# Performance work log

Hardware: AMD Instinct MI355X
Metric: run time of the kernel (lower is better)

Reference implementation:

```python
import jax, jax.numpy as jnp
import numpy as np

B = 2048        # batch
D_IN = 512      # input_dim
H = 768         # hidden_dim
A = 5001        # num_atoms
RULE_LEN = 4
N_DATA = 56000.0


def setup_inputs() -> dict:
    key = jax.random.key(0)
    ks = jax.random.split(key, 24)
    def w(k, shape, fan):
        return (jax.random.normal(k, shape, jnp.float32) / np.sqrt(fan)).astype(jnp.float32)
    return {
        'x': jax.random.normal(ks[0], (B, D_IN), jnp.float32),
        'x_mask': jax.random.randint(ks[1], (B, A), 0, 2, jnp.int32),
        # linear_base: Linear(512,768) ReLU Linear(768,768) ReLU Linear(768,768)
        'W1': w(ks[2], (H, D_IN), D_IN), 'b1': jnp.zeros((H,), jnp.float32),
        'W2': w(ks[3], (H, H), H),       'b2': jnp.zeros((H,), jnp.float32),
        'W3': w(ks[4], (H, H), H),       'b3': jnp.zeros((H,), jnp.float32),
        # single-layer GRU (input H, hidden H); gates ordered r,z,n as in torch
        'W_ih': w(ks[5], (3 * H, H), H), 'b_ih': jnp.zeros((3 * H,), jnp.float32),
        'W_hh': w(ks[6], (3 * H, H), H), 'b_hh': jnp.zeros((3 * H,), jnp.float32),
        # gru_head: Linear(H, num_atoms)
        'Wh': w(ks[7], (A, H), H), 'bh': jnp.zeros((A,), jnp.float32),
        # atom embedding table
        'ae_weight': jax.random.normal(ks[8], (A, H), jnp.float32) * 0.02,
        # stand-in consequent estimator heads (mu, coverage)
        'w_mu': w(ks[9], (H, 1), H),  'b_mu': jnp.zeros((1,), jnp.float32),
        'w_cov': w(ks[10], (H, 1), H), 'b_cov': jnp.zeros((1,), jnp.float32),
        'alpha': jnp.ones((1,), jnp.float32),
    }


def _gru_step(xt, h, W_ih, b_ih, W_hh, b_hh):
    gi = xt @ W_ih.T + b_ih
    gh = h @ W_hh.T + b_hh
    i_r, i_z, i_n = jnp.split(gi, 3, axis=-1)
    h_r, h_z, h_n = jnp.split(gh, 3, axis=-1)
    r = jax.nn.sigmoid(i_r + h_r)
    z = jax.nn.sigmoid(i_z + h_z)
    n = jnp.tanh(i_n + r * h_n)
    return (1.0 - z) * n + z * h


def reference(x, x_mask, W1, b1, W2, b2, W3, b3, W_ih, b_ih, W_hh, b_hh,
              Wh, bh, ae_weight, w_mu, b_mu, w_cov, b_cov, alpha):
    # base (dnn) encoder -> cls embedding [B, H]
    cls = jax.nn.relu(x @ W1.T + b1)
    cls = jax.nn.relu(cls @ W2.T + b2)
    cls = cls @ W3.T + b3

    ae_det = jax.lax.stop_gradient(ae_weight)  # ae.weight is always detached in the original
    mask = x_mask.astype(jnp.float32)
    h = jnp.zeros_like(cls)
    cur = cls
    probs = []
    idx = None
    gkey = jax.random.key(42)
    batch_idx = jnp.arange(cls.shape[0])

    for j in range(RULE_LEN):
        h = _gru_step(cur, h, W_ih, b_ih, W_hh, b_hh)  # dropout = identity (eval)
        logits = h @ Wh.T + bh  # [B, A]
        if j == 0:
            row_zero = jnp.sum(mask, axis=1) == 0.0
            mask = mask.at[:, 0].set(jnp.where(row_zero, 1.0, mask[:, 0]))
        else:
            mask = jnp.where((idx == 0)[:, None], 0.0, mask)
            mask = mask.at[:, 0].set(1.0)
        masked = jnp.where(mask > 0.0, logits, -jnp.inf)
        # gumbel-softmax, tau=1, hard=True (straight-through)
        u = jax.random.uniform(jax.random.fold_in(gkey, j), masked.shape,
                               jnp.float32, 1e-6, 1.0 - 1e-6)
        g = -jnp.log(-jnp.log(u))
        y_soft = jax.nn.softmax(masked + g, axis=1)
        idx = jnp.argmax(y_soft, axis=1)
        y_hard = jax.nn.one_hot(idx, A, dtype=y_soft.dtype)
        prob = y_hard + y_soft - jax.lax.stop_gradient(y_soft)
        probs.append(prob)
        # scatter zero at the selected atom so it can't repeat
        mask = mask.at[batch_idx, idx].set(0.0)
        cur = cls + prob @ ae_det  # [B, H]

    atom_prob = jnp.stack(probs, axis=1)  # [B, rule_len, A]
    atoms = jnp.einsum('bra,ad->brd', atom_prob, ae_det)  # [B, rule_len, H]

    # stand-in consequent estimator: (mu, coverage) from summed atoms
    a = jnp.sum(atoms, axis=1)
    mu = jax.nn.sigmoid(a @ w_mu + b_mu)[:, 0]
    coverage = jax.nn.sigmoid(a @ w_cov + b_cov)[:, 0]

    n = coverage * N_DATA
    inv = alpha[0] / n
    pp = (mu + inv) / (1.0 + 2.0 * inv)
    cp = jnp.stack([1.0 - pp, pp], axis=-1)  # [B, 2]
    out = jnp.log(cp)  # head=1 -> mean over heads is identity
    return (out, atom_prob, cp)
```

## Files before the change

kernel.cpp:

```cpp
#include <hip/hip_runtime.h>
#include <stdint.h>
#include <math.h>

#define B_    2048
#define DIN_  512
#define H_    768
#define G3_   2304
#define A_    5001
#define APAD_ 5120
#define RL_   4
#define NDATA_ 56000.0f

typedef _Float16 f16x8 __attribute__((ext_vector_type(8)));
typedef _Float16 f16x4 __attribute__((ext_vector_type(4)));
typedef float    f32x4 __attribute__((ext_vector_type(4)));

__host__ __device__ __forceinline__ void threefry2x32(
    uint32_t k0, uint32_t k1, uint32_t x0, uint32_t x1,
    uint32_t* o0, uint32_t* o1)
{
  const uint32_t ks2 = k0 ^ k1 ^ 0x1BD11BDAu;
#define TF_R(r) { x0 += x1; x1 = (x1 << (r)) | (x1 >> (32 - (r))); x1 ^= x0; }
  x0 += k0; x1 += k1;
  TF_R(13) TF_R(15) TF_R(26) TF_R(6)
  x0 += k1;  x1 += ks2 + 1u;
  TF_R(17) TF_R(29) TF_R(16) TF_R(24)
  x0 += ks2; x1 += k0 + 2u;
  TF_R(13) TF_R(15) TF_R(26) TF_R(6)
  x0 += k0;  x1 += k1 + 3u;
  TF_R(17) TF_R(29) TF_R(16) TF_R(24)
  x0 += k1;  x1 += ks2 + 4u;
  TF_R(13) TF_R(15) TF_R(26) TF_R(6)
  x0 += ks2; x1 += k0 + 5u;
#undef TF_R
  *o0 = x0; *o1 = x1;
}

__device__ __forceinline__ float gumbel_for(uint32_t k0, uint32_t k1, uint32_t n)
{
  uint32_t o0, o1;
  threefry2x32(k0, k1, 0u, n, &o0, &o1);
  const uint32_t bits = o0 ^ o1;
  const float f = __uint_as_float((bits >> 9) | 0x3f800000u);
  const float minv = 1e-6f;
  const float maxv = 1.0f - 1e-6f;
  const float span = maxv - minv;
  float u = __fmul_rn(f, span);
  u = __fadd_rn(u, minv);
  u = __fsub_rn(u, span);
  u = fmaxf(minv, u);
  return -logf(-logf(u));
}

struct HL { _Float16 h, l; };
__device__ __forceinline__ HL split64(float v)
{
  HL r;
  const float s = v * 64.f;
  r.h = (_Float16)s;
  r.l = (_Float16)(s - (float)r.h);
  return r;
}

__device__ __forceinline__ void gload16(const void* g, void* l)
{
  __builtin_amdgcn_global_load_lds(
      (const __attribute__((address_space(1))) void*)g,
      (__attribute__((address_space(3))) void*)l, 16, 0, 0);
}

struct PSJobs {
  const float* src[7];
  _Float16* hi[7];
  _Float16* lo[7];
  int R[7]; int K[7]; int trans[7];
  int cum[8];
};

__global__ __launch_bounds__(256)
void presplit_all(PSJobs J)
{
  const int g = blockIdx.x * 256 + threadIdx.x;
  if (g >= J.cum[7]) return;
  int j = 0;
  while (g >= J.cum[j + 1]) ++j;
  const int i = g - J.cum[j];
  const int K = J.K[j];
  const int e = i * 4;
  const int row = e / K;
  const int col = e - row * K;
  float4 f = make_float4(0.f, 0.f, 0.f, 0.f);
  if (J.trans[j]) {
    const int R = J.R[j];
    f.x = J.src[j][(size_t)(col + 0) * R + row];
    f.y = J.src[j][(size_t)(col + 1) * R + row];
    f.z = J.src[j][(size_t)(col + 2) * R + row];
    f.w = J.src[j][(size_t)(col + 3) * R + row];
  } else if (row < J.R[j]) {
    f = *(const float4*)(J.src[j] + (size_t)row * K + col);
  }
  const HL s0 = split64(f.x), s1 = split64(f.y);
  const HL s2 = split64(f.z), s3 = split64(f.w);
  const f16x4 hv = {s0.h, s1.h, s2.h, s3.h};
  ((f16x4*)J.hi[j])[i] = hv;
  if (J.lo[j]) {
    const f16x4 lv = {s0.l, s1.l, s2.l, s3.l};
    ((f16x4*)J.lo[j])[i] = lv;
  }
}

__global__ __launch_bounds__(256)
void prep_k(const int* __restrict__ xmask, uint8_t* __restrict__ mask,
            const float* __restrict__ Wh, float* __restrict__ wmaxsq,
            const float* __restrict__ x, _Float16* __restrict__ xh,
            _Float16* __restrict__ xl, const float* __restrict__ Wih,
            const float* __restrict__ b3, const float* __restrict__ bih,
            float* __restrict__ bprime)
{
  const int blk = blockIdx.x, tid = threadIdx.x;
  const int XB = (B_ * DIN_ / 4 + 255) / 256;
  __shared__ float redf[256];
  __shared__ int   redi[256];
  if (blk < B_) {
    const int b = blk;
    int s = 0;
    for (int a = tid; a < A_; a += 256) {
      const int m = (xmask[(size_t)b * A_ + a] != 0) ? 1 : 0;
      mask[(size_t)b * A_ + a] = (uint8_t)m;
      s += m;
    }
    redi[tid] = s; __syncthreads();
    for (int t = 128; t > 0; t >>= 1) {
      if (tid < t) redi[tid] += redi[tid + t];
      __syncthreads();
    }
    if (tid == 0 && redi[0] == 0) mask[(size_t)b * A_] = 1;
  } else if (blk < B_ + A_) {
    const int a = blk - B_;
    float p = 0.f;
    for (int d = tid; d < H_; d += 256) {
      const float w = Wh[(size_t)a * H_ + d];
      p += w * w;
    }
    redf[tid] = p; __syncthreads();
    for (int t = 128; t > 0; t >>= 1) {
      if (tid < t) redf[tid] += redf[tid + t];
      __syncthreads();
    }
    if (tid == 0) atomicMax((int*)wmaxsq, __float_as_int(redf[0]));
  } else if (blk < B_ + A_ + XB) {
    const int i = (blk - B_ - A_) * 256 + tid;
    const int n4 = B_ * DIN_ / 4;
    if (i < n4) {
      const float4 f = ((const float4*)x)[i];
      const HL s0 = split64(f.x), s1 = split64(f.y);
      const HL s2 = split64(f.z), s3 = split64(f.w);
      const f16x4 hv = {s0.h, s1.h, s2.h, s3.h};
      const f16x4 lv = {s0.l, s1.l, s2.l, s3.l};
      ((f16x4*)xh)[i] = hv;
      ((f16x4*)xl)[i] = lv;
    }
  } else {
    const int n = blk - B_ - A_ - XB;
    float p = 0.f;
    for (int d = tid; d < H_; d += 256)
      p += Wih[(size_t)n * H_ + d] * b3[d];
    redf[tid] = p; __syncthreads();
    for (int t = 128; t > 0; t >>= 1) {
      if (tid < t) redf[tid] += redf[tid + t];
      __syncthreads();
    }
    if (tid == 0) bprime[n] = redf[0] + bih[n];
  }
}

struct GJob {
  const _Float16 *Ah, *Al, *Bh, *Bl;
  const float* bias;
  float* C;
  _Float16 *Ch, *Cl;
  int M, K, ldc, n0, Nv;
  int npass, act, wsplit, gum;
};
struct GArgs { GJob j[3]; int sx1, sx2; uint32_t k0, k1; };

__global__ __launch_bounds__(256)
void gemm2job(GArgs P)
{
  __shared__ _Float16 sA[2][128 * 32];
  __shared__ _Float16 sB[2][128 * 32];

  const int bx = blockIdx.x;
  const int jid = (bx < P.sx1) ? 0 : ((bx < P.sx2) ? 1 : 2);
  const GJob J = P.j[jid];
  const int bxx = bx - ((jid == 0) ? 0 : ((jid == 1) ? P.sx1 : P.sx2));
  const int bm = blockIdx.y * 128;
  if (bm >= J.M) return;
  const int bn = J.n0 + bxx * 128;

  const int tid = threadIdx.x;
  const int lane = tid & 63, wave = tid >> 6;
  const int wx = wave & 1, wy = wave >> 1;
  const int q = lane >> 4, mr = lane & 15;
  const int K = J.K;
  const int np3 = (J.npass == 3);

  f32x4 acc[4][4];
#pragma unroll
  for (int i = 0; i < 4; ++i)
#pragma unroll
    for (int j = 0; j < 4; ++j) acc[i][j] = (f32x4)0.f;

  const int abase = (wy * 64 + mr) * 32 + q * 8;
  const int bbase = (wx * 64 + mr) * 32 + q * 8;

  if (np3) {
    auto stage = [&](int k0) {
#pragma unroll
      for (int t = 0; t < 2; ++t) {
        const int c = wave * 2 + t;
        const int row = c * 16 + (lane >> 2);
        const int kc = (lane & 3) * 8;
        const size_t ga = (size_t)(bm + row) * K + k0 + kc;
        const size_t gb = (size_t)(bn + row) * K + k0 + kc;
        gload16(J.Ah + ga, &sA[0][c * 512]);
        gload16(J.Bh + gb, &sB[0][c * 512]);
        gload16(J.Al + ga, &sA[1][c * 512]);
        gload16(J.Bl + gb, &sB[1][c * 512]);
      }
    };
    stage(0);
    const int T = K / 32;
    for (int t = 0; t < T; ++t) {
      __syncthreads();
      f16x8 ah[4], al[4], bhv[4], blv[4];
#pragma unroll
      for (int mi = 0; mi < 4; ++mi) {
        ah[mi]  = *(const f16x8*)&sA[0][abase + mi * 512];
        bhv[mi] = *(const f16x8*)&sB[0][bbase + mi * 512];
        al[mi]  = *(const f16x8*)&sA[1][abase + mi * 512];
        blv[mi] = *(const f16x8*)&sB[1][bbase + mi * 512];
      }
      __syncthreads();
      if (t + 1 < T) stage((t + 1) * 32);
#pragma unroll
      for (int ni = 0; ni < 4; ++ni)
#pragma unroll
        for (int mi = 0; mi < 4; ++mi) {
          acc[mi][ni] = __builtin_amdgcn_mfma_f32_16x16x32_f16(ah[mi], bhv[ni], acc[mi][ni], 0, 0, 0);
          acc[mi][ni] = __builtin_amdgcn_mfma_f32_16x16x32_f16(al[mi], bhv[ni], acc[mi][ni], 0, 0, 0);
          acc[mi][ni] = __builtin_amdgcn_mfma_f32_16x16x32_f16(ah[mi], blv[ni], acc[mi][ni], 0, 0, 0);
        }
    }
  } else {
    auto stage64 = [&](int k0) {
#pragma unroll
      for (int t = 0; t < 2; ++t) {
        const int c = wave * 2 + t;
        const int row = c * 16 + (lane >> 2);
        const int kc = (lane & 3) * 8;
        const size_t ga = (size_t)(bm + row) * K + k0 + kc;
        const size_t gb = (size_t)(bn + row) * K + k0 + kc;
        gload16(J.Ah + ga, &sA[0][c * 512]);
        gload16(J.Bh + gb, &sB[0][c * 512]);
        gload16(J.Ah + ga + 32, &sA[1][c * 512]);
        gload16(J.Bh + gb + 32, &sB[1][c * 512]);
      }
    };
    stage64(0);
    const int T2 = K / 64;
    for (int t = 0; t < T2; ++t) {
      __syncthreads();
      f16x8 a0[4], b0[4];
#pragma unroll
      for (int mi = 0; mi < 4; ++mi) {
        a0[mi] = *(const f16x8*)&sA[0][abase + mi * 512];
        b0[mi] = *(const f16x8*)&sB[0][bbase + mi * 512];
      }
#pragma unroll
      for (int ni = 0; ni < 4; ++ni)
#pragma unroll
        for (int mi = 0; mi < 4; ++mi)
          acc[mi][ni] = __builtin_amdgcn_mfma_f32_16x16x32_f16(a0[mi], b0[ni], acc[mi][ni], 0, 0, 0);
      f16x8 a1[4], b1[4];
#pragma unroll
      for (int mi = 0; mi < 4; ++mi) {
        a1[mi] = *(const f16x8*)&sA[1][abase + mi * 512];
        b1[mi] = *(const f16x8*)&sB[1][bbase + mi * 512];
      }
      __syncthreads();
      if (t + 1 < T2) stage64((t + 1) * 64);
#pragma unroll
      for (int ni = 0; ni < 4; ++ni)
#pragma unroll
        for (int mi = 0; mi < 4; ++mi)
          acc[mi][ni] = __builtin_amdgcn_mfma_f32_16x16x32_f16(a1[mi], b1[ni], acc[mi][ni], 0, 0, 0);
    }
  }

  const float sc = 1.f / 4096.f;
#pragma unroll
  for (int ni = 0; ni < 4; ++ni) {
    const int n = bn + wx * 64 + ni * 16 + mr;
    if (n >= J.Nv) continue;
    const float bv = J.bias ? J.bias[n] : 0.f;
#pragma unroll
    for (int mi = 0; mi < 4; ++mi) {
      const int m0 = bm + wy * 64 + mi * 16 + q * 4;
#pragma unroll
      for (int r = 0; r < 4; ++r) {
        const int m = m0 + r;
        float v = acc[mi][ni][r] * sc + bv;
        if (J.act) v = fmaxf(v, 0.f);
        if (J.gum) v += gumbel_for(P.k0, P.k1, (uint32_t)(m * J.ldc + n));
        const size_t off = (size_t)m * J.ldc + n;
        if (J.C) J.C[off] = v;
        if (J.wsplit) {
          const HL s = split64(v);
          J.Ch[off] = s.h;
          J.Cl[off] = s.l;
        }
      }
    }
  }
}

__global__ __launch_bounds__(256)
void gru_elem(const float* __restrict__ gi, const float* __restrict__ bhh,
              float* __restrict__ h, _Float16* __restrict__ hh_,
              _Float16* __restrict__ hl_)
{
  const int i = blockIdx.x * 256 + threadIdx.x;
  if (i >= B_ * H_) return;
  const int b = i / H_;
  const int d = i - b * H_;
  const float* gib = gi + (size_t)b * G3_;
  const float ir = gib[d], iz = gib[H_ + d], in_ = gib[2 * H_ + d];
  const float hr = bhh[d], hz = bhh[H_ + d], hn = bhh[2 * H_ + d];
  const float r = 1.f / (1.f + expf(-(ir + hr)));
  const float z = 1.f / (1.f + expf(-(iz + hz)));
  const float n = tanhf(in_ + r * hn);
  const float hv = (1.f - z) * n;
  h[i] = hv;
  const HL s = split64(hv);
  hh_[i] = s.h; hl_[i] = s.l;
}

__global__ __launch_bounds__(256)
void select_step(const float* __restrict__ v, uint8_t* __restrict__ mask,
                 int* __restrict__ idxs, const float* __restrict__ giCls,
                 const float* __restrict__ AeWih, float* __restrict__ atomp,
                 float* __restrict__ hbuf, const float* __restrict__ WhF,
                 const float* __restrict__ bh, const float* __restrict__ wmaxsq,
                 const float* __restrict__ gh, const float* __restrict__ bhh,
                 _Float16* __restrict__ hh_, _Float16* __restrict__ hl_,
                 uint32_t k0, uint32_t k1, int step)
{
  const int b = blockIdx.x, tid = threadIdx.x;
  uint8_t* mrow = mask + (size_t)b * A_;
  __shared__ float hsh[H_];
  __shared__ float sv[256];
  __shared__ int   si[256];
  __shared__ int   s_list[64];
  __shared__ int   s_n;
  __shared__ int   s_sel;

  float hp = 0.f;
  for (int d = tid; d < H_; d += 256) {
    const float t = hbuf[(size_t)b * H_ + d];
    hsh[d] = t; hp += t * t;
  }
  sv[tid] = hp; __syncthreads();
  for (int t = 128; t > 0; t >>= 1) {
    if (tid < t) sv[tid] += sv[tid + t];
    __syncthreads();
  }
  const float hn2 = sv[0];
  __syncthreads();

  if (step > 0) {
    const int prev = idxs[(step - 1) * B_ + b];
    if (prev == 0)
      for (int a = tid; a < A_; a += 256) mrow[a] = 0;
    __syncthreads();
    if (tid == 0) mrow[0] = 1;
  }
  if (tid == 0) s_n = 0;
  __syncthreads();

  const float* vrow = v + (size_t)b * A_;
  float bv = -INFINITY; int bi = A_;
  for (int a = tid; a < A_; a += 256) {
    const float val = mrow[a] ? vrow[a] : -INFINITY;
    if (val > bv) { bv = val; bi = a; }
  }
  sv[tid] = bv; si[tid] = bi; __syncthreads();
  for (int t = 128; t > 0; t >>= 1) {
    if (tid < t) {
      const float v2 = sv[tid + t]; const int i2 = si[tid + t];
      if (v2 > sv[tid] || (v2 == sv[tid] && i2 < si[tid])) { sv[tid] = v2; si[tid] = i2; }
    }
    __syncthreads();
  }
  const float amax = sv[0];
  __syncthreads();

  const float delta = 2.0f * 0.0009765625f * sqrtf(hn2 * wmaxsq[0]);
  const float thr = amax - 2.f * delta;

  for (int a = tid; a < A_; a += 256)
    if (mrow[a] && vrow[a] >= thr) {
      const int p = atomicAdd(&s_n, 1);
      if (p < 64) s_list[p] = a;
    }
  __syncthreads();
  const int nc = (s_n < 64) ? s_n : 64;

  const uint32_t nbase = (uint32_t)b * (uint32_t)A_;
  float best = -INFINITY; int bestA = A_;
  for (int c = 0; c < nc; ++c) {
    const int a = s_list[c];
    const float* wr = WhF + (size_t)a * H_;
    float p = 0.f;
    for (int d = tid; d < H_; d += 256) p += hsh[d] * wr[d];
    sv[tid] = p; __syncthreads();
    for (int t = 128; t > 0; t >>= 1) {
      if (tid < t) sv[tid] += sv[tid + t];
      __syncthreads();
    }
    if (tid == 0) {
      const float ev = sv[0] + bh[a] + gumbel_for(k0, k1, nbase + (uint32_t)a);
      if (ev > best || (ev == best && a < bestA)) { best = ev; bestA = a; }
    }
    __syncthreads();
  }
  if (tid == 0) {
    s_sel = bestA;
    mrow[bestA] = 0;
    idxs[step * B_ + b] = bestA;
    atomp[(size_t)b * (RL_ * A_) + (size_t)step * A_ + bestA] = 1.0f;
  }
  __syncthreads();

  if (step < RL_ - 1) {
    const int sel = s_sel;
    const float* ar = AeWih + (size_t)sel * G3_;
    const float* gr = giCls + (size_t)b * G3_;
    const float* ghb = gh + (size_t)b * G3_;
    for (int d = tid; d < H_; d += 256) {
      const float g0 = gr[d] + ar[d];
      const float g1 = gr[H_ + d] + ar[H_ + d];
      const float g2 = gr[2 * H_ + d] + ar[2 * H_ + d];
      const float r = 1.f / (1.f + expf(-(g0 + ghb[d])));
      const float z = 1.f / (1.f + expf(-(g1 + ghb[H_ + d])));
      const float n = tanhf(g2 + r * ghb[2 * H_ + d]);
      const float hv = (1.f - z) * n + z * hsh[d];
      hbuf[(size_t)b * H_ + d] = hv;
      const HL s = split64(hv);
      hh_[(size_t)b * H_ + d] = s.h;
      hl_[(size_t)b * H_ + d] = s.l;
    }
  }
}

__global__ __launch_bounds__(256)
void head_k(const int* __restrict__ idxs, const float* __restrict__ ae,
            const float* __restrict__ w_mu, const float* __restrict__ b_mu,
            const float* __restrict__ w_cov, const float* __restrict__ b_cov,
            const float* __restrict__ alpha, float* __restrict__ outf)
{
  const int b = blockIdx.x, tid = threadIdx.x;
  const int i0 = idxs[0 * B_ + b], i1 = idxs[1 * B_ + b];
  const int i2 = idxs[2 * B_ + b], i3 = idxs[3 * B_ + b];
  const float* r0 = ae + (size_t)i0 * H_;
  const float* r1 = ae + (size_t)i1 * H_;
  const float* r2 = ae + (size_t)i2 * H_;
  const float* r3 = ae + (size_t)i3 * H_;
  float pmu = 0.f, pcv = 0.f;
  for (int d = tid; d < H_; d += 256) {
    const float a = r0[d] + r1[d] + r2[d] + r3[d];
    pmu += a * w_mu[d];
    pcv += a * w_cov[d];
  }
  __shared__ float smu[256], scv[256];
  smu[tid] = pmu; scv[tid] = pcv;
  __syncthreads();
  for (int s = 128; s > 0; s >>= 1) {
    if (tid < s) { smu[tid] += smu[tid + s]; scv[tid] += scv[tid + s]; }
    __syncthreads();
  }
  if (tid == 0) {
    const float mu = 1.f / (1.f + expf(-(smu[0] + b_mu[0])));
    const float cv = 1.f / (1.f + expf(-(scv[0] + b_cov[0])));
    const float n = cv * NDATA_;
    const float inv = alpha[0] / n;
    const float pp = (mu + inv) / (1.f + 2.f * inv);
    outf[2 * b + 0] = logf(1.f - pp);
    outf[2 * b + 1] = logf(pp);
    float* cp = outf + 2 * B_ + (size_t)B_ * RL_ * A_;
    cp[2 * b + 0] = 1.f - pp;
    cp[2 * b + 1] = pp;
  }
}

extern "C" void kernel_launch(void* const* d_in, const int* in_sizes, int n_in,
                              void* d_out, int out_size, void* d_ws, size_t ws_size,
                              hipStream_t stream)
{
  const float* x     = (const float*)d_in[0];
  const int*   xmask = (const int*)d_in[1];
  const float* W1 = (const float*)d_in[2];  const float* b1 = (const float*)d_in[3];
  const float* W2 = (const float*)d_in[4];  const float* b2 = (const float*)d_in[5];
  const float* W3 = (const float*)d_in[6];  const float* b3 = (const float*)d_in[7];
  const float* Wih = (const float*)d_in[8]; const float* bih = (const float*)d_in[9];
  const float* Whh = (const float*)d_in[10];const float* bhh = (const float*)d_in[11];
  const float* Wh = (const float*)d_in[12]; const float* bh = (const float*)d_in[13];
  const float* ae = (const float*)d_in[14];
  const float* w_mu = (const float*)d_in[15];  const float* b_mu = (const float*)d_in[16];
  const float* w_cov = (const float*)d_in[17]; const float* b_cov = (const float*)d_in[18];
  const float* alpha = (const float*)d_in[19];

  char* ws = (char*)d_ws;
  size_t off = 0;
  auto alloc = [&](size_t bytes) -> void* {
    void* p = ws + off;
    off += (bytes + 255) & ~(size_t)255;
    return p;
  };
  float* hbuf   = (float*)alloc((size_t)B_ * H_ * 4);
  float* giCls  = (float*)alloc((size_t)B_ * G3_ * 4);
  float* gh     = (float*)alloc((size_t)B_ * G3_ * 4);
  float* vbuf   = (float*)alloc((size_t)B_ * A_ * 4);
  float* AeWih  = (float*)alloc((size_t)APAD_ * G3_ * 4);
  uint8_t* mask = (uint8_t*)alloc((size_t)B_ * A_);
  int* idxs     = (int*)alloc((size_t)RL_ * B_ * 4);
  _Float16* hh_ = (_Float16*)alloc((size_t)B_ * H_ * 2);
  _Float16* hl_ = (_Float16*)alloc((size_t)B_ * H_ * 2);
  _Float16* xh  = (_Float16*)alloc((size_t)B_ * DIN_ * 2);
  _Float16* xl  = (_Float16*)alloc((size_t)B_ * DIN_ * 2);
  _Float16* t1h = (_Float16*)alloc((size_t)B_ * H_ * 2);
  _Float16* t1l = (_Float16*)alloc((size_t)B_ * H_ * 2);
  _Float16* t2h = (_Float16*)alloc((size_t)B_ * H_ * 2);
  _Float16* t2l = (_Float16*)alloc((size_t)B_ * H_ * 2);
  _Float16* w1h = (_Float16*)alloc((size_t)H_ * DIN_ * 2);
  _Float16* w1l = (_Float16*)alloc((size_t)H_ * DIN_ * 2);
  _Float16* w2h = (_Float16*)alloc((size_t)H_ * H_ * 2);
  _Float16* w2l = (_Float16*)alloc((size_t)H_ * H_ * 2);
  _Float16* w3th = (_Float16*)alloc((size_t)H_ * H_ * 2);
  _Float16* w3tl = (_Float16*)alloc((size_t)H_ * H_ * 2);
  _Float16* wihh = (_Float16*)alloc((size_t)G3_ * H_ * 2);
  _Float16* wihl = (_Float16*)alloc((size_t)G3_ * H_ * 2);
  _Float16* whhh = (_Float16*)alloc((size_t)G3_ * H_ * 2);
  _Float16* whhl = (_Float16*)alloc((size_t)G3_ * H_ * 2);
  _Float16* whhi = (_Float16*)alloc((size_t)APAD_ * H_ * 2);
  _Float16* aeh  = (_Float16*)alloc((size_t)APAD_ * H_ * 2);
  _Float16* ael  = (_Float16*)alloc((size_t)APAD_ * H_ * 2);
  _Float16* wph  = (_Float16*)alloc((size_t)G3_ * H_ * 2);
  _Float16* wpl  = (_Float16*)alloc((size_t)G3_ * H_ * 2);
  float* bprime = (float*)alloc((size_t)G3_ * 4);
  float* wmaxsq = (float*)alloc(4);

  float* outf  = (float*)d_out;
  float* atomp = outf + 2 * B_;

  (void)hipMemsetAsync(d_out, 0, (size_t)out_size * sizeof(float), stream);
  (void)hipMemsetAsync(wmaxsq, 0, 4, stream);

  PSJobs J;
  const float* srcs[7] = {W1, W2, W3, Wih, Whh, Wh, ae};
  _Float16* his[7] = {w1h, w2h, w3th, wihh, whhh, whhi, aeh};
  _Float16* los[7] = {w1l, w2l, w3tl, wihl, whhl, nullptr, ael};
  const int Rs[7]    = {H_, H_, H_, G3_, G3_, A_, A_};
  const int Rpads[7] = {H_, H_, H_, G3_, G3_, APAD_, APAD_};
  const int Ks[7]    = {DIN_, H_, H_, H_, H_, H_, H_};
  const int Trs[7]   = {0, 0, 1, 0, 0, 0, 0};
  J.cum[0] = 0;
  for (int j = 0; j < 7; ++j) {
    J.src[j] = srcs[j]; J.hi[j] = his[j]; J.lo[j] = los[j];
    J.R[j] = Rs[j]; J.K[j] = Ks[j]; J.trans[j] = Trs[j];
    J.cum[j + 1] = J.cum[j] + Rpads[j] * Ks[j] / 4;
  }
  presplit_all<<<(J.cum[7] + 255) / 256, 256, 0, stream>>>(J);

  const int XB = (B_ * DIN_ / 4 + 255) / 256;
  prep_k<<<B_ + A_ + XB + G3_, 256, 0, stream>>>(
      xmask, mask, Wh, wmaxsq, x, xh, xl, Wih, b3, bih, bprime);

  auto mkjob = [](const _Float16* Ah, const _Float16* Al, const _Float16* Bh,
                  const _Float16* Bl, const float* bias, float* C,
                  _Float16* Ch, _Float16* Cl, int M, int K, int ldc,
                  int n0, int Nv, int npass, int act, int wsplit, int gum) {
    GJob g; g.Ah = Ah; g.Al = Al; g.Bh = Bh; g.Bl = Bl; g.bias = bias;
    g.C = C; g.Ch = Ch; g.Cl = Cl; g.M = M; g.K = K; g.ldc = ldc;
    g.n0 = n0; g.Nv = Nv; g.npass = npass; g.act = act; g.wsplit = wsplit;
    g.gum = gum;
    return g;
  };
  auto aejob = [&](int t0) {
    return mkjob(aeh, ael, wihh, wihl, nullptr, AeWih, nullptr, nullptr,
                 APAD_, H_, G3_, t0 * 128, G3_, 3, 0, 0, 0);
  };

  {
    GArgs P;
    P.j[0] = mkjob(xh, xl, w1h, w1l, b1, nullptr, t1h, t1l,
                   B_, DIN_, H_, 0, H_, 3, 1, 1, 0);
    P.j[1] = mkjob(wihh, wihl, w3th, w3tl, nullptr, nullptr, wph, wpl,
                   G3_, H_, H_, 0, H_, 3, 0, 1, 0);
    P.j[2] = aejob(0);
    P.sx1 = H_ / 128; P.sx2 = H_ / 128 + H_ / 128; P.k0 = 0; P.k1 = 0;
    gemm2job<<<dim3(P.sx2 + 6, APAD_ / 128), 256, 0, stream>>>(P);
  }
  {
    GArgs P;
    P.j[0] = mkjob(t1h, t1l, w2h, w2l, b2, nullptr, t2h, t2l,
                   B_, H_, H_, 0, H_, 3, 1, 1, 0);
    P.j[1] = aejob(6);
    P.j[2] = P.j[1];
    P.sx1 = H_ / 128; P.sx2 = H_ / 128 + 6; P.k0 = 0; P.k1 = 0;
    gemm2job<<<dim3(P.sx2, APAD_ / 128), 256, 0, stream>>>(P);
  }
  {
    GArgs P;
    P.j[0] = mkjob(t2h, t2l, wph, wpl, bprime, giCls, nullptr, nullptr,
                   B_, H_, G3_, 0, G3_, 3, 0, 0, 0);
    P.j[1] = aejob(12);
    P.j[2] = P.j[1];
    P.sx1 = G3_ / 128; P.sx2 = G3_ / 128 + 6; P.k0 = 0; P.k1 = 0;
    gemm2job<<<dim3(P.sx2, APAD_ / 128), 256, 0, stream>>>(P);
  }

  uint32_t fk0[RL_], fk1[RL_];
  for (int j = 0; j < RL_; ++j)
    threefry2x32(0u, 42u, 0u, (uint32_t)j, &fk0[j], &fk1[j]);

  gru_elem<<<(B_ * H_ + 255) / 256, 256, 0, stream>>>(giCls, bhh, hbuf, hh_, hl_);

  for (int j = 0; j < RL_; ++j) {
    GArgs P;
    P.j[0] = mkjob(hh_, nullptr, whhi, nullptr, bh, vbuf, nullptr, nullptr,
                   B_, H_, A_, 0, A_, 1, 0, 0, 1);
    const int gx0 = APAD_ / 128;
    int gx = gx0;
    if (j < RL_ - 1) {
      P.j[1] = mkjob(hh_, hl_, whhh, whhl, bhh, gh, nullptr, nullptr,
                     B_, H_, G3_, 0, G3_, 3, 0, 0, 0);
      gx += G3_ / 128;
    } else {
      P.j[1] = P.j[0];
    }
    P.j[2] = P.j[1];
    P.sx1 = gx0; P.sx2 = gx; P.k0 = fk0[j]; P.k1 = fk1[j];
    gemm2job<<<dim3(gx, B_ / 128), 256, 0, stream>>>(P);

    select_step<<<B_, 256, 0, stream>>>(vbuf, mask, idxs, giCls, AeWih, atomp,
                                        hbuf, Wh, bh, wmaxsq, gh, bhh, hh_, hl_,
                                        fk0[j], fk1[j], j);
  }

  head_k<<<B_, 256, 0, stream>>>(idxs, ae, w_mu, b_mu, w_cov, b_cov, alpha, outf);
}
```

Baseline: 981.3 us.

## Fuse masked row-max into logits GEMM epilogue and swap grid axes

The Gumbel logits GEMM epilogue now applies the atom mask, writes -inf for masked entries and computes a per-row maximum through an LDS atomicMax followed by a global atomicMax on order-preserving encoded floats. select_step reads that precomputed row max, dropping its full argmax pass over the mask and logits, and now updates the mask after selection rather than before. Grid dimensions are swapped so blockIdx.x walks M tiles, which changes block scheduling order and L2 reuse of weight tiles. The cost is extra mask reads and atomics in the GEMM epilogue, plus a rowmax buffer that must be reset between steps.

After: 932.9 us. 4.9% less time.

```diff
diff --git a/kernel.cpp b/kernel.cpp
--- a/kernel.cpp
+++ b/kernel.cpp
@@ -60,6 +60,17 @@
   r.h = (_Float16)s;
   r.l = (_Float16)(s - (float)r.h);
   return r;
+}
+
+__device__ __forceinline__ uint32_t encmax(float f)
+{
+  const uint32_t b = __float_as_uint(f);
+  return (b & 0x80000000u) ? ~b : (b | 0x80000000u);
+}
+__device__ __forceinline__ float decmax(uint32_t u)
+{
+  const uint32_t b = (u & 0x80000000u) ? (u & 0x7FFFFFFFu) : ~u;
+  return __uint_as_float(b);
 }
 
 __device__ __forceinline__ void gload16(const void* g, void* l)
@@ -179,6 +190,8 @@
   const float* bias;
   float* C;
   _Float16 *Ch, *Cl;
+  const uint8_t* mask;
+  uint32_t* rowmax;
   int M, K, ldc, n0, Nv;
   int npass, act, wsplit, gum;
 };
@@ -190,11 +203,11 @@
   __shared__ _Float16 sA[2][128 * 32];
   __shared__ _Float16 sB[2][128 * 32];
 
-  const int bx = blockIdx.x;
-  const int jid = (bx < P.sx1) ? 0 : ((bx < P.sx2) ? 1 : 2);
+  const int by = blockIdx.y;
+  const int jid = (by < P.sx1) ? 0 : ((by < P.sx2) ? 1 : 2);
   const GJob J = P.j[jid];
-  const int bxx = bx - ((jid == 0) ? 0 : ((jid == 1) ? P.sx1 : P.sx2));
-  const int bm = blockIdx.y * 128;
+  const int bxx = by - ((jid == 0) ? 0 : ((jid == 1) ? P.sx1 : P.sx2));
+  const int bm = blockIdx.x * 128;
   if (bm >= J.M) return;
   const int bn = J.n0 + bxx * 128;
 
@@ -299,6 +312,12 @@
   }
 
   const float sc = 1.f / 4096.f;
+  float lm[4][4];
+#pragma unroll
+  for (int mi = 0; mi < 4; ++mi)
+#pragma unroll
+    for (int r = 0; r < 4; ++r) lm[mi][r] = -INFINITY;
+
 #pragma unroll
   for (int ni = 0; ni < 4; ++ni) {
     const int n = bn + wx * 64 + ni * 16 + mr;
@@ -312,9 +331,15 @@
         const int m = m0 + r;
         float v = acc[mi][ni][r] * sc + bv;
         if (J.act) v = fmaxf(v, 0.f);
-        if (J.gum) v += gumbel_for(P.k0, P.k1, (uint32_t)(m * J.ldc + n));
         const size_t off = (size_t)m * J.ldc + n;
-        if (J.C) J.C[off] = v;
+        if (J.gum) {
+          v += gumbel_for(P.k0, P.k1, (uint32_t)(m * J.ldc + n));
+          const bool ok = J.mask[off] != 0;
+          if (ok && v > lm[mi][r]) lm[mi][r] = v;
+          J.C[off] = ok ? v : -INFINITY;
+        } else {
+          if (J.C) J.C[off] = v;
+        }
         if (J.wsplit) {
           const HL s = split64(v);
           J.Ch[off] = s.h;
@@ -323,17 +348,32 @@
       }
     }
   }
+
+  if (J.gum) {
+    uint32_t* rmx = (uint32_t*)&sA[0][0];
+    __syncthreads();
+    if (tid < 128) rmx[tid] = 0u;
+    __syncthreads();
+#pragma unroll
+    for (int mi = 0; mi < 4; ++mi)
+#pragma unroll
+      for (int r = 0; r < 4; ++r)
+        atomicMax(&rmx[wy * 64 + mi * 16 + q * 4 + r], encmax(lm[mi][r]));
+    __syncthreads();
+    if (tid < 128) atomicMax(J.rowmax + bm + tid, rmx[tid]);
+  }
 }
 
 __global__ __launch_bounds__(256)
 void gru_elem(const float* __restrict__ gi, const float* __restrict__ bhh,
               float* __restrict__ h, _Float16* __restrict__ hh_,
-              _Float16* __restrict__ hl_)
+              _Float16* __restrict__ hl_, uint32_t* __restrict__ rowmax)
 {
   const int i = blockIdx.x * 256 + threadIdx.x;
   if (i >= B_ * H_) return;
   const int b = i / H_;
   const int d = i - b * H_;
+  if (d == 0) rowmax[b] = 0u;
   const float* gib = gi + (size_t)b * G3_;
   const float ir = gib[d], iz = gib[H_ + d], in_ = gib[2 * H_ + d];
   const float hr = bhh[d], hz = bhh[H_ + d], hn = bhh[2 * H_ + d];
@@ -354,13 +394,13 @@
                  const float* __restrict__ bh, const float* __restrict__ wmaxsq,
                  const float* __restrict__ gh, const float* __restrict__ bhh,
                  _Float16* __restrict__ hh_, _Float16* __restrict__ hl_,
+                 uint32_t* __restrict__ rowmax,
                  uint32_t k0, uint32_t k1, int step)
 {
   const int b = blockIdx.x, tid = threadIdx.x;
   uint8_t* mrow = mask + (size_t)b * A_;
   __shared__ float hsh[H_];
   __shared__ float sv[256];
-  __shared__ int   si[256];
   __shared__ int   s_list[64];
   __shared__ int   s_n;
   __shared__ int   s_sel;
@@ -370,7 +410,9 @@
     const float t = hbuf[(size_t)b * H_ + d];
     hsh[d] = t; hp += t * t;
   }
-  sv[tid] = hp; __syncthreads();
+  sv[tid] = hp;
+  if (tid == 0) s_n = 0;
+  __syncthreads();
   for (int t = 128; t > 0; t >>= 1) {
     if (tid < t) sv[tid] += sv[tid + t];
     __syncthreads();
@@ -378,38 +420,13 @@
   const float hn2 = sv[0];
   __syncthreads();
 
-  if (step > 0) {
-    const int prev = idxs[(step - 1) * B_ + b];
-    if (prev == 0)
-      for (int a = tid; a < A_; a += 256) mrow[a] = 0;
-    __syncthreads();
-    if (tid == 0) mrow[0] = 1;
-  }
-  if (tid == 0) s_n = 0;
-  __syncthreads();
-
-  const float* vrow = v + (size_t)b * A_;
-  float bv = -INFINITY; int bi = A_;
-  for (int a = tid; a < A_; a += 256) {
-    const float val = mrow[a] ? vrow[a] : -INFINITY;
-    if (val > bv) { bv = val; bi = a; }
-  }
-  sv[tid] = bv; si[tid] = bi; __syncthreads();
-  for (int t = 128; t > 0; t >>= 1) {
-    if (tid < t) {
-      const float v2 = sv[tid + t]; const int i2 = si[tid + t];
-      if (v2 > sv[tid] || (v2 == sv[tid] && i2 < si[tid])) { sv[tid] = v2; si[tid] = i2; }
-    }
-    __syncthreads();
-  }
-  const float amax = sv[0];
-  __syncthreads();
-
+  const float amax = decmax(rowmax[b]);
   const float delta = 2.0f * 0.0009765625f * sqrtf(hn2 * wmaxsq[0]);
   const float thr = amax - 2.f * delta;
 
+  const float* vrow = v + (size_t)b * A_;
   for (int a = tid; a < A_; a += 256)
-    if (mrow[a] && vrow[a] >= thr) {
+    if (vrow[a] >= thr) {
       const int p = atomicAdd(&s_n, 1);
       if (p < 64) s_list[p] = a;
     }
@@ -436,14 +453,22 @@
   }
   if (tid == 0) {
     s_sel = bestA;
-    mrow[bestA] = 0;
     idxs[step * B_ + b] = bestA;
     atomp[(size_t)b * (RL_ * A_) + (size_t)step * A_ + bestA] = 1.0f;
   }
   __syncthreads();
+  const int sel = s_sel;
 
   if (step < RL_ - 1) {
-    const int sel = s_sel;
+    if (sel == 0) {
+      for (int a = tid; a < A_; a += 256) mrow[a] = 0;
+    }
+    __syncthreads();
+    if (tid == 0) {
+      if (sel != 0) mrow[sel] = 0;
+      mrow[0] = 1;
+      rowmax[b] = 0u;
+    }
     const float* ar = AeWih + (size_t)sel * G3_;
     const float* gr = giCls + (size_t)b * G3_;
     const float* ghb = gh + (size_t)b * G3_;
@@ -534,6 +559,7 @@
   float* AeWih  = (float*)alloc((size_t)APAD_ * G3_ * 4);
   uint8_t* mask = (uint8_t*)alloc((size_t)B_ * A_);
   int* idxs     = (int*)alloc((size_t)RL_ * B_ * 4);
+  uint32_t* rowmax = (uint32_t*)alloc((size_t)B_ * 4);
   _Float16* hh_ = (_Float16*)alloc((size_t)B_ * H_ * 2);
   _Float16* hl_ = (_Float16*)alloc((size_t)B_ * H_ * 2);
   _Float16* xh  = (_Float16*)alloc((size_t)B_ * DIN_ * 2);
@@ -591,7 +617,8 @@
                   _Float16* Ch, _Float16* Cl, int M, int K, int ldc,
                   int n0, int Nv, int npass, int act, int wsplit, int gum) {
     GJob g; g.Ah = Ah; g.Al = Al; g.Bh = Bh; g.Bl = Bl; g.bias = bias;
-    g.C = C; g.Ch = Ch; g.Cl = Cl; g.M = M; g.K = K; g.ldc = ldc;
+    g.C = C; g.Ch = Ch; g.Cl = Cl; g.mask = nullptr; g.rowmax = nullptr;
+    g.M = M; g.K = K; g.ldc = ldc;
     g.n0 = n0; g.Nv = Nv; g.npass = npass; g.act = act; g.wsplit = wsplit;
     g.gum = gum;
     return g;
@@ -609,7 +636,7 @@
                    G3_, H_, H_, 0, H_, 3, 0, 1, 0);
     P.j[2] = aejob(0);
     P.sx1 = H_ / 128; P.sx2 = H_ / 128 + H_ / 128; P.k0 = 0; P.k1 = 0;
-    gemm2job<<<dim3(P.sx2 + 6, APAD_ / 128), 256, 0, stream>>>(P);
+    gemm2job<<<dim3(APAD_ / 128, P.sx2 + 6), 256, 0, stream>>>(P);
   }
   {
     GArgs P;
@@ -618,7 +645,7 @@
     P.j[1] = aejob(6);
     P.j[2] = P.j[1];
     P.sx1 = H_ / 128; P.sx2 = H_ / 128 + 6; P.k0 = 0; P.k1 = 0;
-    gemm2job<<<dim3(P.sx2, APAD_ / 128), 256, 0, stream>>>(P);
+    gemm2job<<<dim3(APAD_ / 128, P.sx2), 256, 0, stream>>>(P);
   }
   {
     GArgs P;
@@ -627,19 +654,21 @@
     P.j[1] = aejob(12);
     P.j[2] = P.j[1];
     P.sx1 = G3_ / 128; P.sx2 = G3_ / 128 + 6; P.k0 = 0; P.k1 = 0;
-    gemm2job<<<dim3(P.sx2, APAD_ / 128), 256, 0, stream>>>(P);
+    gemm2job<<<dim3(APAD_ / 128, P.sx2), 256, 0, stream>>>(P);
   }
 
   uint32_t fk0[RL_], fk1[RL_];
   for (int j = 0; j < RL_; ++j)
     threefry2x32(0u, 42u, 0u, (uint32_t)j, &fk0[j], &fk1[j]);
 
-  gru_elem<<<(B_ * H_ + 255) / 256, 256, 0, stream>>>(giCls, bhh, hbuf, hh_, hl_);
+  gru_elem<<<(B_ * H_ + 255) / 256, 256, 0, stream>>>(giCls, bhh, hbuf, hh_,
+                                                      hl_, rowmax);
 
   for (int j = 0; j < RL_; ++j) {
     GArgs P;
     P.j[0] = mkjob(hh_, nullptr, whhi, nullptr, bh, vbuf, nullptr, nullptr,
                    B_, H_, A_, 0, A_, 1, 0, 0, 1);
+    P.j[0].mask = mask; P.j[0].rowmax = rowmax;
     const int gx0 = APAD_ / 128;
     int gx = gx0;
     if (j < RL_ - 1) {
@@ -651,11 +680,11 @@
     }
     P.j[2] = P.j[1];
     P.sx1 = gx0; P.sx2 = gx; P.k0 = fk0[j]; P.k1 = fk1[j];
-    gemm2job<<<dim3(gx, B_ / 128), 256, 0, stream>>>(P);
+    gemm2job<<<dim3(B_ / 128, gx), 256, 0, stream>>>(P);
 
     select_step<<<B_, 256, 0, stream>>>(vbuf, mask, idxs, giCls, AeWih, atomp,
                                         hbuf, Wh, bh, wmaxsq, gh, bhh, hh_, hl_,
-                                        fk0[j], fk1[j], j);
+                                        rowmax, fk0[j], fk1[j], j);
   }
 
   head_k<<<B_, 256, 0, stream>>>(idxs, ae, w_mu, b_mu, w_cov, b_cov, alpha, outf);
```
